# Kernel tuning notes

Hardware: AMD Instinct MI355X
Metric: run time of the kernel (lower is better)

Reference implementation:

```python
import jax, jax.numpy as jnp
import numpy as np

N_HEAD = 16

def setup_inputs() -> dict:
    key = jax.random.key(0)
    ks = jax.random.split(key, 6)
    B, S, T, D = 4, 1024, 576, 1024
    std = 0.02
    return {
        "x": jax.random.normal(ks[0], (B, S, D), jnp.float32),
        "encoder_output": jax.random.normal(ks[1], (B, T, D), jnp.float32),
        "w_attn": jax.random.normal(ks[2], (D, 3 * D), jnp.float32) * std,
        "b_attn": jnp.zeros((3 * D,), jnp.float32),
        "w_vis": jax.random.normal(ks[3], (D, D), jnp.float32) * std,
        "b_vis": jnp.zeros((D,), jnp.float32),
        "w_proj": jax.random.normal(ks[4], (D, D), jnp.float32) * std,
        "b_proj": jnp.zeros((D,), jnp.float32),
    }

def _split_heads(t):
    # [B, L, D] -> [B, H, L, d_head]
    B, L, D = t.shape
    return t.reshape(B, L, N_HEAD, D // N_HEAD).transpose(0, 2, 1, 3)

def reference(x, encoder_output, w_attn, b_attn, w_vis, b_vis, w_proj, b_proj):
    B, S, D = x.shape
    # c_attn: qkv projection of text; only q is actually used downstream
    qkv = x @ w_attn + b_attn                      # [B, S, 3D]
    q = _split_heads(qkv[..., :D])                 # [B, H, S, dh]
    # visual_proj: single projection used as BOTH key and value
    enc = encoder_output @ w_vis + b_vis           # [B, T, D]
    kv = _split_heads(enc)                         # [B, H, T, dh]
    dh = D // N_HEAD
    # scaled dot-product cross-attention (scale=True -> / sqrt(d_head))
    w = jnp.einsum("bhsd,bhtd->bhst", q, kv) / jnp.sqrt(jnp.float32(dh))
    w = jax.nn.softmax(w, axis=-1)                 # attn_dropout=0 (eval)
    a = jnp.einsum("bhst,bhtd->bhsd", w, kv)       # [B, H, S, dh]
    a = a.transpose(0, 2, 1, 3).reshape(B, S, D)   # merge heads
    out = a @ w_proj + b_proj                      # resid_dropout=0 (eval)
    return out
```

## Files before the change

### kernel.cpp

```cpp
#include <hip/hip_runtime.h>
#include <math.h>

#define D_MODEL 1024
#define NHEAD   16
#define DH      64
#define BATCH   4
#define SEQ     1024
#define TKV     576
#define MQ      (BATCH * SEQ)
#define MKV     (BATCH * TKV)
#define NT      (TKV / 64)

typedef __attribute__((ext_vector_type(8))) short bf16x8;
typedef __attribute__((ext_vector_type(4))) float f32x4;

__device__ __forceinline__ unsigned short f2bf(float x) {
    unsigned int u = __float_as_uint(x);
    unsigned int r = (u + 0x7FFFu + ((u >> 16) & 1u)) >> 16;
    return (unsigned short)r;
}
__device__ __forceinline__ float bf2f(unsigned short b) {
    return __uint_as_float((unsigned int)b << 16);
}
__device__ __forceinline__ void split2(float x, unsigned short& h, unsigned short& l) {
    h = f2bf(x);
    l = f2bf(x - bf2f(h));
}

__device__ __forceinline__ void async_copy16(const void* g, void* l) {
    auto gp = (const __attribute__((address_space(1))) unsigned int*)(g);
    auto lp = (__attribute__((address_space(3))) unsigned int*)(l);
    __builtin_amdgcn_global_load_lds(gp, lp, 16, 0, 0);
}

__global__ __launch_bounds__(256) void split_rm(
    const float* __restrict__ in,
    unsigned short* __restrict__ oh, unsigned short* __restrict__ ol)
{
    const size_t i = (size_t)blockIdx.x * 256 + threadIdx.x;
    const float4 v = reinterpret_cast<const float4*>(in)[i];
    ushort4 h, l;
    split2(v.x, h.x, l.x);
    split2(v.y, h.y, l.y);
    split2(v.z, h.z, l.z);
    split2(v.w, h.w, l.w);
    reinterpret_cast<ushort4*>(oh)[i] = h;
    reinterpret_cast<ushort4*>(ol)[i] = l;
}

__global__ __launch_bounds__(256) void split_tr(
    const float* __restrict__ W, int ld,
    unsigned short* __restrict__ th, unsigned short* __restrict__ tl)
{
    __shared__ float sh[32][33];
    const int k0 = blockIdx.x * 32;
    const int n0 = blockIdx.y * 32;
    const int t  = threadIdx.x;
    const int r  = t >> 3;
    const int c4 = (t & 7) * 4;

    const float4 v = *reinterpret_cast<const float4*>(&W[(size_t)(k0 + r) * ld + n0 + c4]);
    sh[r][c4 + 0] = v.x;
    sh[r][c4 + 1] = v.y;
    sh[r][c4 + 2] = v.z;
    sh[r][c4 + 3] = v.w;
    __syncthreads();

    ushort4 h, l;
    split2(sh[c4 + 0][r], h.x, l.x);
    split2(sh[c4 + 1][r], h.y, l.y);
    split2(sh[c4 + 2][r], h.z, l.z);
    split2(sh[c4 + 3][r], h.w, l.w);
    *reinterpret_cast<ushort4*>(&th[(size_t)(n0 + r) * 1024 + k0 + c4]) = h;
    *reinterpret_cast<ushort4*>(&tl[(size_t)(n0 + r) * 1024 + k0 + c4]) = l;
}

__global__ __launch_bounds__(256) void transpose_hl(
    const unsigned short* __restrict__ kvh, const unsigned short* __restrict__ kvl,
    unsigned short* __restrict__ kvth, unsigned short* __restrict__ kvtl)
{
    __shared__ __align__(16) unsigned short th_[64][72];
    __shared__ __align__(16) unsigned short tl_[64][72];
    const int tid = threadIdx.x;
    const int t0  = blockIdx.x * 64;
    const int bh  = blockIdx.y;
    const int b   = bh >> 4;
    const int h   = bh & 15;

#pragma unroll
    for (int p = 0; p < 2; ++p) {
        const int idx = p * 256 + tid;
        const int rr  = idx >> 3;
        const int c   = idx & 7;
        const size_t src = (size_t)(b * TKV + t0 + rr) * 1024 + h * DH + c * 8;
        const bf16x8 vh = *(const bf16x8*)&kvh[src];
        const bf16x8 vl = *(const bf16x8*)&kvl[src];
#pragma unroll
        for (int e = 0; e < 8; ++e) {
            th_[c * 8 + e][rr] = (unsigned short)vh[e];
            tl_[c * 8 + e][rr] = (unsigned short)vl[e];
        }
    }
    __syncthreads();

#pragma unroll
    for (int p = 0; p < 2; ++p) {
        const int idx = p * 256 + tid;
        const int d   = idx >> 3;
        const int c2  = idx & 7;
        const size_t dst = (size_t)(bh * 64 + d) * TKV + t0 + c2 * 8;
        *(bf16x8*)&kvth[dst] = *(const bf16x8*)&th_[d][c2 * 8];
        *(bf16x8*)&kvtl[dst] = *(const bf16x8*)&tl_[d][c2 * 8];
    }
}

template<bool BF16OUT>
__global__ __launch_bounds__(256) void gemm_split_mfma(
    const unsigned short* __restrict__ Ah, const unsigned short* __restrict__ Al,
    const unsigned short* __restrict__ Bth, const unsigned short* __restrict__ Btl,
    const float* __restrict__ bias,
    float* __restrict__ C,
    unsigned short* __restrict__ Ch, unsigned short* __restrict__ Cl,
    int M)
{
    __shared__ unsigned short lds[2][16384];

    const int tid  = threadIdx.x;
    const int lane = tid & 63;
    const int wv   = tid >> 6;

    const int nwg = (gridDim.y << 3);
    const int lin = blockIdx.y * 8 + blockIdx.x;
    const int cpx = nwg >> 3;
    const int swz = (lin & 7) * cpx + (lin >> 3);
    const int brow = (swz >> 3) * 128;
    const int bcol = (swz & 7) * 128;

    const int wr = (wv >> 1) * 64;
    const int wc = (wv & 1) * 64;
    const int lr = lane & 15;
    const int kg = lane >> 4;

    f32x4 acc[4][4];
#pragma unroll
    for (int i = 0; i < 4; ++i)
#pragma unroll
        for (int j = 0; j < 4; ++j) acc[i][j] = (f32x4){0.f, 0.f, 0.f, 0.f};

    auto stage = [&](int buf, int k0) {
#pragma unroll
        for (int i = 0; i < 2; ++i) {
            const int ci = i * 256 + tid;
            const int r  = ci >> 2;
            const int c  = ci & 3;
            const size_t aoff = (size_t)(brow + r) * 1024 + k0 + c * 8;
            const size_t boff = (size_t)(bcol + r) * 1024 + k0 + c * 8;
            char* ldst = (char*)&lds[buf][0] + i * 4096 + wv * 1024;
            async_copy16(Ah  + aoff, ldst);
            async_copy16(Al  + aoff, ldst + 8192);
            async_copy16(Bth + boff, ldst + 16384);
            async_copy16(Btl + boff, ldst + 24576);
        }
    };

    stage(0, 0);
    __syncthreads();

    int cur = 0;
    for (int kt = 0; kt < 32; ++kt) {
        stage(cur ^ 1, ((kt + 1) & 31) << 5);

        const unsigned short* lAh = lds[cur];
        const unsigned short* lAl = lds[cur] + 4096;
        const unsigned short* lBh = lds[cur] + 8192;
        const unsigned short* lBl = lds[cur] + 12288;

        bf16x8 afh[4], afl[4], bfh[4], bfl[4];
#pragma unroll
        for (int f = 0; f < 4; ++f) {
            const int mb = (wr + f * 16 + lr) * 64 + kg * 16;
            const int nb = (wc + f * 16 + lr) * 64 + kg * 16;
            afh[f] = *(const bf16x8*)((const char*)lAh + mb);
            afl[f] = *(const bf16x8*)((const char*)lAl + mb);
            bfh[f] = *(const bf16x8*)((const char*)lBh + nb);
            bfl[f] = *(const bf16x8*)((const char*)lBl + nb);
        }

#pragma unroll
        for (int mf = 0; mf < 4; ++mf)
#pragma unroll
            for (int nf = 0; nf < 4; ++nf) {
                acc[mf][nf] = __builtin_amdgcn_mfma_f32_16x16x32_bf16(afh[mf], bfh[nf], acc[mf][nf], 0, 0, 0);
                acc[mf][nf] = __builtin_amdgcn_mfma_f32_16x16x32_bf16(afh[mf], bfl[nf], acc[mf][nf], 0, 0, 0);
                acc[mf][nf] = __builtin_amdgcn_mfma_f32_16x16x32_bf16(afl[mf], bfh[nf], acc[mf][nf], 0, 0, 0);
            }
        __syncthreads();
        cur ^= 1;
    }

#pragma unroll
    for (int mf = 0; mf < 4; ++mf)
#pragma unroll
        for (int nf = 0; nf < 4; ++nf)
#pragma unroll
            for (int j = 0; j < 4; ++j) {
                const int row = brow + wr + mf * 16 + kg * 4 + j;
                const int col = bcol + wc + nf * 16 + lr;
                const float v = acc[mf][nf][j] + bias[col];
                if constexpr (BF16OUT) {
                    unsigned short hh, ll;
                    split2(v, hh, ll);
                    Ch[(size_t)row * 1024 + col] = hh;
                    Cl[(size_t)row * 1024 + col] = ll;
                } else {
                    C[(size_t)row * 1024 + col] = v;
                }
            }
}

__global__ __launch_bounds__(256, 2) void attn_mfma(
    const unsigned short* __restrict__ qh, const unsigned short* __restrict__ ql,
    const unsigned short* __restrict__ kvh, const unsigned short* __restrict__ kvl,
    const unsigned short* __restrict__ kvth, const unsigned short* __restrict__ kvtl,
    unsigned short* __restrict__ ah, unsigned short* __restrict__ al)
{
    __shared__ __align__(16) unsigned short kh_s[64][64],  kl_s[64][64];
    __shared__ __align__(16) unsigned short vth_s[64][64], vtl_s[64][64];
    __shared__ __align__(16) unsigned short ph_s[4][32][64], pl_s[4][32][64];

    const int tid  = threadIdx.x;
    const int lane = tid & 63;
    const int w    = tid >> 6;
    const int lr   = lane & 15;
    const int kg   = lane >> 4;
    const int s0   = blockIdx.x * 128;
    const int bh   = blockIdx.y;
    const int b    = bh >> 4;
    const int h    = bh & 15;

    const int r0 = tid >> 3;
    const int c0 = tid & 7;

    bf16x8 qhf[2][2], qlf[2][2];
#pragma unroll
    for (int g = 0; g < 2; ++g) {
        const size_t qoff = (size_t)(b * SEQ + s0 + w * 32 + g * 16 + lr) * 1024 + h * DH;
#pragma unroll
        for (int c = 0; c < 2; ++c) {
            qhf[g][c] = *(const bf16x8*)&qh[qoff + c * 32 + kg * 8];
            qlf[g][c] = *(const bf16x8*)&ql[qoff + c * 32 + kg * 8];
        }
    }

    f32x4 oacc[2][4];
#pragma unroll
    for (int g = 0; g < 2; ++g)
#pragma unroll
        for (int nf = 0; nf < 4; ++nf) oacc[g][nf] = (f32x4){0.f, 0.f, 0.f, 0.f};
    float m2[2][4], lsum[2][4];
#pragma unroll
    for (int g = 0; g < 2; ++g)
#pragma unroll
        for (int j = 0; j < 4; ++j) { m2[g][j] = -INFINITY; lsum[g][j] = 0.f; }

    bf16x8 nkh[2], nkl[2], nvh[2], nvl[2];

    auto ld_tile = [&](int it) {
#pragma unroll
        for (int i = 0; i < 2; ++i) {
            const int rr = r0 + i * 32;
            const size_t kvo = (size_t)(b * TKV + it * 64 + rr) * 1024 + h * DH + c0 * 8;
            const size_t vto = (size_t)(bh * 64 + rr) * TKV + it * 64 + c0 * 8;
            nkh[i] = *(const bf16x8*)&kvh[kvo];
            nkl[i] = *(const bf16x8*)&kvl[kvo];
            nvh[i] = *(const bf16x8*)&kvth[vto];
            nvl[i] = *(const bf16x8*)&kvtl[vto];
        }
    };
    auto st_tile = [&]() {
#pragma unroll
        for (int i = 0; i < 2; ++i) {
            const int rr = r0 + i * 32;
            const int sc = (c0 ^ (rr & 7)) * 8;
            *(bf16x8*)&kh_s[rr][sc]  = nkh[i];
            *(bf16x8*)&kl_s[rr][sc]  = nkl[i];
            *(bf16x8*)&vth_s[rr][sc] = nvh[i];
            *(bf16x8*)&vtl_s[rr][sc] = nvl[i];
        }
    };

    ld_tile(0);
    st_tile();
    __syncthreads();

    const float SC2 = 0.125f * 1.44269504089f;

    for (int it = 0; it < NT; ++it) {
        if (it + 1 < NT) ld_tile(it + 1);

        f32x4 sacc[2][4];
#pragma unroll
        for (int g = 0; g < 2; ++g)
#pragma unroll
            for (int nf = 0; nf < 4; ++nf) sacc[g][nf] = (f32x4){0.f, 0.f, 0.f, 0.f};
#pragma unroll
        for (int c = 0; c < 2; ++c) {
            const int ch = (((c << 2) | kg) ^ (lr & 7)) << 3;
#pragma unroll
            for (int nf = 0; nf < 4; ++nf) {
                const bf16x8 bhf = *(const bf16x8*)&kh_s[nf * 16 + lr][ch];
                const bf16x8 blf = *(const bf16x8*)&kl_s[nf * 16 + lr][ch];
#pragma unroll
                for (int g = 0; g < 2; ++g) {
                    sacc[g][nf] = __builtin_amdgcn_mfma_f32_16x16x32_bf16(qhf[g][c], bhf, sacc[g][nf], 0, 0, 0);
                    sacc[g][nf] = __builtin_amdgcn_mfma_f32_16x16x32_bf16(qhf[g][c], blf, sacc[g][nf], 0, 0, 0);
                    sacc[g][nf] = __builtin_amdgcn_mfma_f32_16x16x32_bf16(qlf[g][c], bhf, sacc[g][nf], 0, 0, 0);
                }
            }
        }

#pragma unroll
        for (int g = 0; g < 2; ++g)
#pragma unroll
            for (int j = 0; j < 4; ++j) {
                const float s0v = sacc[g][0][j] * SC2;
                const float s1v = sacc[g][1][j] * SC2;
                const float s2v = sacc[g][2][j] * SC2;
                const float s3v = sacc[g][3][j] * SC2;
                float mx = fmaxf(fmaxf(s0v, s1v), fmaxf(s2v, s3v));
                mx = fmaxf(mx, __shfl_xor(mx, 1));
                mx = fmaxf(mx, __shfl_xor(mx, 2));
                mx = fmaxf(mx, __shfl_xor(mx, 4));
                mx = fmaxf(mx, __shfl_xor(mx, 8));
                const float mnew = fmaxf(m2[g][j], mx);
                const float corr = exp2f(m2[g][j] - mnew);
                const float p0 = exp2f(s0v - mnew);
                const float p1 = exp2f(s1v - mnew);
                const float p2 = exp2f(s2v - mnew);
                const float p3 = exp2f(s3v - mnew);
                float ps = p0 + p1 + p2 + p3;
                ps += __shfl_xor(ps, 1);
                ps += __shfl_xor(ps, 2);
                ps += __shfl_xor(ps, 4);
                ps += __shfl_xor(ps, 8);
                lsum[g][j] = lsum[g][j] * corr + ps;
                m2[g][j] = mnew;
#pragma unroll
                for (int nf = 0; nf < 4; ++nf) oacc[g][nf][j] *= corr;
                const int prow = g * 16 + kg * 4 + j;
                const int key  = prow & 7;
                const int lo3  = lr & 7;
                const int hi1  = lr >> 3;
                unsigned short hh, ll;
                split2(p0, hh, ll);
                ph_s[w][prow][((0 + hi1) ^ key) * 8 + lo3] = hh;
                pl_s[w][prow][((0 + hi1) ^ key) * 8 + lo3] = ll;
                split2(p1, hh, ll);
                ph_s[w][prow][((2 + hi1) ^ key) * 8 + lo3] = hh;
                pl_s[w][prow][((2 + hi1) ^ key) * 8 + lo3] = ll;
                split2(p2, hh, ll);
                ph_s[w][prow][((4 + hi1) ^ key) * 8 + lo3] = hh;
                pl_s[w][prow][((4 + hi1) ^ key) * 8 + lo3] = ll;
                split2(p3, hh, ll);
                ph_s[w][prow][((6 + hi1) ^ key) * 8 + lo3] = hh;
                pl_s[w][prow][((6 + hi1) ^ key) * 8 + lo3] = ll;
            }

#pragma unroll
        for (int c = 0; c < 2; ++c) {
            const int ch = (((c << 2) | kg) ^ (lr & 7)) << 3;
            bf16x8 pha[2], pla[2];
#pragma unroll
            for (int g = 0; g < 2; ++g) {
                pha[g] = *(const bf16x8*)&ph_s[w][g * 16 + lr][ch];
                pla[g] = *(const bf16x8*)&pl_s[w][g * 16 + lr][ch];
            }
#pragma unroll
            for (int nf = 0; nf < 4; ++nf) {
                const bf16x8 vhf = *(const bf16x8*)&vth_s[nf * 16 + lr][ch];
                const bf16x8 vlf = *(const bf16x8*)&vtl_s[nf * 16 + lr][ch];
#pragma unroll
                for (int g = 0; g < 2; ++g) {
                    oacc[g][nf] = __builtin_amdgcn_mfma_f32_16x16x32_bf16(pha[g], vhf, oacc[g][nf], 0, 0, 0);
                    oacc[g][nf] = __builtin_amdgcn_mfma_f32_16x16x32_bf16(pha[g], vlf, oacc[g][nf], 0, 0, 0);
                    oacc[g][nf] = __builtin_amdgcn_mfma_f32_16x16x32_bf16(pla[g], vhf, oacc[g][nf], 0, 0, 0);
                }
            }
        }

        __syncthreads();
        if (it + 1 < NT) st_tile();
        __syncthreads();
    }

#pragma unroll
    for (int g = 0; g < 2; ++g)
#pragma unroll
        for (int nf = 0; nf < 4; ++nf)
#pragma unroll
            for (int j = 0; j < 4; ++j) {
                const float v = oacc[g][nf][j] / lsum[g][j];
                const int srow = b * SEQ + s0 + w * 32 + g * 16 + kg * 4 + j;
                const int col  = h * DH + nf * 16 + lr;
                unsigned short hh, ll;
                split2(v, hh, ll);
                ah[(size_t)srow * 1024 + col] = hh;
                al[(size_t)srow * 1024 + col] = ll;
            }
}

extern "C" void kernel_launch(void* const* d_in, const int* in_sizes, int n_in,
                              void* d_out, int out_size, void* d_ws, size_t ws_size,
                              hipStream_t stream)
{
    const float* x      = (const float*)d_in[0];
    const float* enc    = (const float*)d_in[1];
    const float* w_attn = (const float*)d_in[2];
    const float* b_attn = (const float*)d_in[3];
    const float* w_vis  = (const float*)d_in[4];
    const float* b_vis  = (const float*)d_in[5];
    const float* w_proj = (const float*)d_in[6];
    const float* b_proj = (const float*)d_in[7];
    float* out = (float*)d_out;

    char* base = (char*)d_ws;
    unsigned short* xh   = (unsigned short*)(base + 0);
    unsigned short* xl   = (unsigned short*)(base + 8388608);
    unsigned short* ench = (unsigned short*)(base + 16777216);
    unsigned short* encl = (unsigned short*)(base + 21495808);
    unsigned short* w1h  = (unsigned short*)(base + 26214400);
    unsigned short* w1l  = (unsigned short*)(base + 28311552);
    unsigned short* w2h  = (unsigned short*)(base + 30408704);
    unsigned short* w2l  = (unsigned short*)(base + 32505856);
    unsigned short* w3h  = (unsigned short*)(base + 34603008);
    unsigned short* w3l  = (unsigned short*)(base + 36700160);
    unsigned short* qh   = (unsigned short*)(base + 38797312);
    unsigned short* ql   = (unsigned short*)(base + 47185920);
    unsigned short* kvh  = (unsigned short*)(base + 55574528);
    unsigned short* kvl  = (unsigned short*)(base + 60293120);
    unsigned short* kvth = (unsigned short*)(base + 0);
    unsigned short* kvtl = (unsigned short*)(base + 4718592);
    unsigned short* atth = (unsigned short*)(base + 16777216);
    unsigned short* attl = (unsigned short*)(base + 26214400);

    split_rm<<<(MQ  * 1024 / 4) / 256, 256, 0, stream>>>(x, xh, xl);
    split_rm<<<(MKV * 1024 / 4) / 256, 256, 0, stream>>>(enc, ench, encl);
    split_tr<<<dim3(32, 32), 256, 0, stream>>>(w_attn, 3 * D_MODEL, w1h, w1l);
    split_tr<<<dim3(32, 32), 256, 0, stream>>>(w_vis,  D_MODEL, w2h, w2l);
    split_tr<<<dim3(32, 32), 256, 0, stream>>>(w_proj, D_MODEL, w3h, w3l);

    gemm_split_mfma<true><<<dim3(8, MQ / 128), 256, 0, stream>>>(
        xh, xl, w1h, w1l, b_attn, nullptr, qh, ql, MQ);
    gemm_split_mfma<true><<<dim3(8, MKV / 128), 256, 0, stream>>>(
        ench, encl, w2h, w2l, b_vis, nullptr, kvh, kvl, MKV);
    transpose_hl<<<dim3(TKV / 64, BATCH * NHEAD), 256, 0, stream>>>(kvh, kvl, kvth, kvtl);
    attn_mfma<<<dim3(SEQ / 128, BATCH * NHEAD), 256, 0, stream>>>(
        qh, ql, kvh, kvl, kvth, kvtl, atth, attl);
    gemm_split_mfma<false><<<dim3(8, MQ / 128), 256, 0, stream>>>(
        atth, attl, w3h, w3l, b_proj, out, nullptr, nullptr, MQ);
}
```

Before: 284.9 us.

## Merge Q/KV projection GEMMs and restructure attention with async LDS staging

Merges the Q and KV projection GEMMs into a single launch so the two fill the GPU together instead of running back to back. The attention kernel is rewritten to stage K and V tiles into LDS with async copies, using a pre-permuted V layout built by the transpose kernel. It computes S^T so softmax probabilities stay in registers instead of going through LDS, and raises occupancy to 3 blocks per CU by shrinking shared memory. The cost is more complex indexing, extra syncs per tile, and a serialized K/V staging order that may expose latency.

```diff
diff --git a/kernel.cpp b/kernel.cpp
--- a/kernel.cpp
+++ b/kernel.cpp
@@ -75,14 +75,15 @@
     *reinterpret_cast<ushort4*>(&tl[(size_t)(n0 + r) * 1024 + k0 + c4]) = l;
 }
 
-__global__ __launch_bounds__(256) void transpose_hl(
+__global__ __launch_bounds__(256) void transpose_perm(
     const unsigned short* __restrict__ kvh, const unsigned short* __restrict__ kvl,
-    unsigned short* __restrict__ kvth, unsigned short* __restrict__ kvtl)
+    unsigned short* __restrict__ vph, unsigned short* __restrict__ vpl)
 {
     __shared__ __align__(16) unsigned short th_[64][72];
     __shared__ __align__(16) unsigned short tl_[64][72];
     const int tid = threadIdx.x;
-    const int t0  = blockIdx.x * 64;
+    const int it  = blockIdx.x;
+    const int t0  = it * 64;
     const int bh  = blockIdx.y;
     const int b   = bh >> 4;
     const int h   = bh & 15;
@@ -107,35 +108,35 @@
     for (int p = 0; p < 2; ++p) {
         const int idx = p * 256 + tid;
         const int d   = idx >> 3;
-        const int c2  = idx & 7;
-        const size_t dst = (size_t)(bh * 64 + d) * TKV + t0 + c2 * 8;
-        *(bf16x8*)&kvth[dst] = *(const bf16x8*)&th_[d][c2 * 8];
-        *(bf16x8*)&kvtl[dst] = *(const bf16x8*)&tl_[d][c2 * 8];
+        const int lc  = idx & 7;
+        const int q   = lc >> 2;
+        const int kg  = lc & 3;
+        const ushort4 a  = *(const ushort4*)&th_[d][32 * q + kg * 4];
+        const ushort4 bb = *(const ushort4*)&th_[d][32 * q + 16 + kg * 4];
+        const ushort4 a2  = *(const ushort4*)&tl_[d][32 * q + kg * 4];
+        const ushort4 bb2 = *(const ushort4*)&tl_[d][32 * q + 16 + kg * 4];
+        bf16x8 oh_, ol_;
+        oh_[0] = (short)a.x;  oh_[1] = (short)a.y;  oh_[2] = (short)a.z;  oh_[3] = (short)a.w;
+        oh_[4] = (short)bb.x; oh_[5] = (short)bb.y; oh_[6] = (short)bb.z; oh_[7] = (short)bb.w;
+        ol_[0] = (short)a2.x;  ol_[1] = (short)a2.y;  ol_[2] = (short)a2.z;  ol_[3] = (short)a2.w;
+        ol_[4] = (short)bb2.x; ol_[5] = (short)bb2.y; ol_[6] = (short)bb2.z; ol_[7] = (short)bb2.w;
+        const size_t dst = ((size_t)(bh * 64 + d) * NT + it) * 64 + lc * 8;
+        *(bf16x8*)&vph[dst] = oh_;
+        *(bf16x8*)&vpl[dst] = ol_;
     }
 }
 
 template<bool BF16OUT>
-__global__ __launch_bounds__(256) void gemm_split_mfma(
-    const unsigned short* __restrict__ Ah, const unsigned short* __restrict__ Al,
-    const unsigned short* __restrict__ Bth, const unsigned short* __restrict__ Btl,
-    const float* __restrict__ bias,
-    float* __restrict__ C,
-    unsigned short* __restrict__ Ch, unsigned short* __restrict__ Cl,
-    int M)
-{
-    __shared__ unsigned short lds[2][16384];
-
+__device__ __forceinline__ void gemm_body(
+    const unsigned short* Ah, const unsigned short* Al,
+    const unsigned short* Bth, const unsigned short* Btl,
+    const float* bias, float* C,
+    unsigned short* Ch, unsigned short* Cl,
+    int brow, int bcol, unsigned short* lds )
+{
     const int tid  = threadIdx.x;
     const int lane = tid & 63;
     const int wv   = tid >> 6;
-
-    const int nwg = (gridDim.y << 3);
-    const int lin = blockIdx.y * 8 + blockIdx.x;
-    const int cpx = nwg >> 3;
-    const int swz = (lin & 7) * cpx + (lin >> 3);
-    const int brow = (swz >> 3) * 128;
-    const int bcol = (swz & 7) * 128;
-
     const int wr = (wv >> 1) * 64;
     const int wc = (wv & 1) * 64;
     const int lr = lane & 15;
@@ -155,7 +156,7 @@
             const int c  = ci & 3;
             const size_t aoff = (size_t)(brow + r) * 1024 + k0 + c * 8;
             const size_t boff = (size_t)(bcol + r) * 1024 + k0 + c * 8;
-            char* ldst = (char*)&lds[buf][0] + i * 4096 + wv * 1024;
+            char* ldst = (char*)lds + buf * 32768 + i * 4096 + wv * 1024;
             async_copy16(Ah  + aoff, ldst);
             async_copy16(Al  + aoff, ldst + 8192);
             async_copy16(Bth + boff, ldst + 16384);
@@ -170,10 +171,10 @@
     for (int kt = 0; kt < 32; ++kt) {
         stage(cur ^ 1, ((kt + 1) & 31) << 5);
 
-        const unsigned short* lAh = lds[cur];
-        const unsigned short* lAl = lds[cur] + 4096;
-        const unsigned short* lBh = lds[cur] + 8192;
-        const unsigned short* lBl = lds[cur] + 12288;
+        const unsigned short* lAh = lds + cur * 16384;
+        const unsigned short* lAl = lAh + 4096;
+        const unsigned short* lBh = lAh + 8192;
+        const unsigned short* lBl = lAh + 12288;
 
         bf16x8 afh[4], afl[4], bfh[4], bfl[4];
 #pragma unroll
@@ -218,15 +219,53 @@
             }
 }
 
-__global__ __launch_bounds__(256, 2) void attn_mfma(
+__global__ __launch_bounds__(256) void gemm_split_mfma_f32(
+    const unsigned short* __restrict__ Ah, const unsigned short* __restrict__ Al,
+    const unsigned short* __restrict__ Bth, const unsigned short* __restrict__ Btl,
+    const float* __restrict__ bias, float* __restrict__ C)
+{
+    __shared__ unsigned short lds[2 * 16384];
+    const int nwg = (gridDim.y << 3);
+    const int lin = blockIdx.y * 8 + blockIdx.x;
+    const int cpx = nwg >> 3;
+    const int swz = (lin & 7) * cpx + (lin >> 3);
+    gemm_body<false>(Ah, Al, Bth, Btl, bias, C, nullptr, nullptr,
+                     (swz >> 3) * 128, (swz & 7) * 128, lds);
+}
+
+__global__ __launch_bounds__(256) void gemm12_split_mfma(
+    const unsigned short* __restrict__ A1h, const unsigned short* __restrict__ A1l,
+    const unsigned short* __restrict__ B1h, const unsigned short* __restrict__ B1l,
+    const float* __restrict__ bias1,
+    unsigned short* __restrict__ C1h, unsigned short* __restrict__ C1l,
+    const unsigned short* __restrict__ A2h, const unsigned short* __restrict__ A2l,
+    const unsigned short* __restrict__ B2h, const unsigned short* __restrict__ B2l,
+    const float* __restrict__ bias2,
+    unsigned short* __restrict__ C2h, unsigned short* __restrict__ C2l)
+{
+    __shared__ unsigned short lds[2 * 16384];
+    const int nwg = (gridDim.y << 3);
+    const int lin = blockIdx.y * 8 + blockIdx.x;
+    const int cpx = nwg >> 3;
+    const int swz = (lin & 7) * cpx + (lin >> 3);
+    const int ridx = swz >> 3;
+    const int bcol = (swz & 7) * 128;
+    if (ridx < 32) {
+        gemm_body<true>(A1h, A1l, B1h, B1l, bias1, nullptr, C1h, C1l,
+                        ridx * 128, bcol, lds);
+    } else {
+        gemm_body<true>(A2h, A2l, B2h, B2l, bias2, nullptr, C2h, C2l,
+                        (ridx - 32) * 128, bcol, lds);
+    }
+}
+
+__global__ __launch_bounds__(256, 3) void attn_mfma(
     const unsigned short* __restrict__ qh, const unsigned short* __restrict__ ql,
     const unsigned short* __restrict__ kvh, const unsigned short* __restrict__ kvl,
-    const unsigned short* __restrict__ kvth, const unsigned short* __restrict__ kvtl,
+    const unsigned short* __restrict__ vph, const unsigned short* __restrict__ vpl,
     unsigned short* __restrict__ ah, unsigned short* __restrict__ al)
 {
-    __shared__ __align__(16) unsigned short kh_s[64][64],  kl_s[64][64];
-    __shared__ __align__(16) unsigned short vth_s[64][64], vtl_s[64][64];
-    __shared__ __align__(16) unsigned short ph_s[4][32][64], pl_s[4][32][64];
+    __shared__ __align__(16) unsigned short smem[4 * 4096];
 
     const int tid  = threadIdx.x;
     const int lane = tid & 63;
@@ -237,9 +276,31 @@
     const int bh   = blockIdx.y;
     const int b    = bh >> 4;
     const int h    = bh & 15;
-
-    const int r0 = tid >> 3;
-    const int c0 = tid & 7;
+    const int rr0  = tid >> 3;
+    const int cc   = tid & 7;
+
+    auto stageK = [&](int it) {
+#pragma unroll
+        for (int i = 0; i < 2; ++i) {
+            const int rr = rr0 + i * 32;
+            const int lc = cc ^ (rr & 7);
+            const size_t src = (size_t)(b * TKV + it * 64 + rr) * 1024 + h * DH + lc * 8;
+            char* dst = (char*)smem + i * 4096 + w * 1024;
+            async_copy16(kvh + src, dst);
+            async_copy16(kvl + src, dst + 8192);
+        }
+    };
+    auto stageV = [&](int it) {
+#pragma unroll
+        for (int i = 0; i < 2; ++i) {
+            const int rr = rr0 + i * 32;
+            const int lc = cc ^ (rr & 7);
+            const size_t src = ((size_t)(bh * 64 + rr) * NT + it) * 64 + lc * 8;
+            char* dst = (char*)smem + 16384 + i * 4096 + w * 1024;
+            async_copy16(vph + src, dst);
+            async_copy16(vpl + src, dst + 8192);
+        }
+    };
 
     bf16x8 qhf[2][2], qlf[2][2];
 #pragma unroll
@@ -256,157 +317,117 @@
 #pragma unroll
     for (int g = 0; g < 2; ++g)
 #pragma unroll
-        for (int nf = 0; nf < 4; ++nf) oacc[g][nf] = (f32x4){0.f, 0.f, 0.f, 0.f};
-    float m2[2][4], lsum[2][4];
-#pragma unroll
-    for (int g = 0; g < 2; ++g)
-#pragma unroll
-        for (int j = 0; j < 4; ++j) { m2[g][j] = -INFINITY; lsum[g][j] = 0.f; }
-
-    bf16x8 nkh[2], nkl[2], nvh[2], nvl[2];
-
-    auto ld_tile = [&](int it) {
-#pragma unroll
-        for (int i = 0; i < 2; ++i) {
-            const int rr = r0 + i * 32;
-            const size_t kvo = (size_t)(b * TKV + it * 64 + rr) * 1024 + h * DH + c0 * 8;
-            const size_t vto = (size_t)(bh * 64 + rr) * TKV + it * 64 + c0 * 8;
-            nkh[i] = *(const bf16x8*)&kvh[kvo];
-            nkl[i] = *(const bf16x8*)&kvl[kvo];
-            nvh[i] = *(const bf16x8*)&kvth[vto];
-            nvl[i] = *(const bf16x8*)&kvtl[vto];
-        }
-    };
-    auto st_tile = [&]() {
-#pragma unroll
-        for (int i = 0; i < 2; ++i) {
-            const int rr = r0 + i * 32;
-            const int sc = (c0 ^ (rr & 7)) * 8;
-            *(bf16x8*)&kh_s[rr][sc]  = nkh[i];
-            *(bf16x8*)&kl_s[rr][sc]  = nkl[i];
-            *(bf16x8*)&vth_s[rr][sc] = nvh[i];
-            *(bf16x8*)&vtl_s[rr][sc] = nvl[i];
-        }
-    };
-
-    ld_tile(0);
-    st_tile();
+        for (int df = 0; df < 4; ++df) oacc[g][df] = (f32x4){0.f, 0.f, 0.f, 0.f};
+    float m2[2]   = {-INFINITY, -INFINITY};
+    float lsum[2] = {0.f, 0.f};
+
+    stageK(0);
+    stageV(0);
     __syncthreads();
 
     const float SC2 = 0.125f * 1.44269504089f;
 
     for (int it = 0; it < NT; ++it) {
-        if (it + 1 < NT) ld_tile(it + 1);
-
         f32x4 sacc[2][4];
 #pragma unroll
         for (int g = 0; g < 2; ++g)
 #pragma unroll
-            for (int nf = 0; nf < 4; ++nf) sacc[g][nf] = (f32x4){0.f, 0.f, 0.f, 0.f};
-#pragma unroll
-        for (int c = 0; c < 2; ++c) {
-            const int ch = (((c << 2) | kg) ^ (lr & 7)) << 3;
-#pragma unroll
-            for (int nf = 0; nf < 4; ++nf) {
-                const bf16x8 bhf = *(const bf16x8*)&kh_s[nf * 16 + lr][ch];
-                const bf16x8 blf = *(const bf16x8*)&kl_s[nf * 16 + lr][ch];
+            for (int kf = 0; kf < 4; ++kf) sacc[g][kf] = (f32x4){0.f, 0.f, 0.f, 0.f};
+#pragma unroll
+        for (int c = 0; c < 2; ++c)
+#pragma unroll
+            for (int kf = 0; kf < 4; ++kf) {
+                const int ka = (kf * 16 + lr) * 128 + ((((c << 2) | kg) ^ (lr & 7)) << 4);
+                const bf16x8 akh = *(const bf16x8*)((const char*)smem + ka);
+                const bf16x8 akl = *(const bf16x8*)((const char*)smem + 8192 + ka);
 #pragma unroll
                 for (int g = 0; g < 2; ++g) {
-                    sacc[g][nf] = __builtin_amdgcn_mfma_f32_16x16x32_bf16(qhf[g][c], bhf, sacc[g][nf], 0, 0, 0);
-                    sacc[g][nf] = __builtin_amdgcn_mfma_f32_16x16x32_bf16(qhf[g][c], blf, sacc[g][nf], 0, 0, 0);
-                    sacc[g][nf] = __builtin_amdgcn_mfma_f32_16x16x32_bf16(qlf[g][c], bhf, sacc[g][nf], 0, 0, 0);
+                    sacc[g][kf] = __builtin_amdgcn_mfma_f32_16x16x32_bf16(akh, qhf[g][c], sacc[g][kf], 0, 0, 0);
+                    sacc[g][kf] = __builtin_amdgcn_mfma_f32_16x16x32_bf16(akh, qlf[g][c], sacc[g][kf], 0, 0, 0);
+                    sacc[g][kf] = __builtin_amdgcn_mfma_f32_16x16x32_bf16(akl, qhf[g][c], sacc[g][kf], 0, 0, 0);
                 }
             }
-        }
-
-#pragma unroll
-        for (int g = 0; g < 2; ++g)
+
+        __syncthreads();
+        if (it + 1 < NT) stageK(it + 1);
+
+        bf16x8 pbh[2][2], pbl[2][2];
+#pragma unroll
+        for (int g = 0; g < 2; ++g) {
+            float p[16];
+            float mx = -INFINITY;
+#pragma unroll
+            for (int kf = 0; kf < 4; ++kf)
+#pragma unroll
+                for (int j = 0; j < 4; ++j) {
+                    p[kf * 4 + j] = sacc[g][kf][j] * SC2;
+                    mx = fmaxf(mx, p[kf * 4 + j]);
+                }
+            mx = fmaxf(mx, __shfl_xor(mx, 16));
+            mx = fmaxf(mx, __shfl_xor(mx, 32));
+            const float mnew = fmaxf(m2[g], mx);
+            const float corr = exp2f(m2[g] - mnew);
+            float ps = 0.f;
+#pragma unroll
+            for (int i = 0; i < 16; ++i) { p[i] = exp2f(p[i] - mnew); ps += p[i]; }
+            ps += __shfl_xor(ps, 16);
+            ps += __shfl_xor(ps, 32);
+            lsum[g] = lsum[g] * corr + ps;
+            m2[g] = mnew;
+#pragma unroll
+            for (int df = 0; df < 4; ++df)
+#pragma unroll
+                for (int j = 0; j < 4; ++j) oacc[g][df][j] *= corr;
+#pragma unroll
+            for (int q = 0; q < 2; ++q) {
+                bf16x8 bh_, bl_;
+#pragma unroll
+                for (int e = 0; e < 8; ++e) {
+                    unsigned short hh, ll;
+                    split2(p[(2 * q + (e >> 2)) * 4 + (e & 3)], hh, ll);
+                    bh_[e] = (short)hh;
+                    bl_[e] = (short)ll;
+                }
+                pbh[g][q] = bh_;
+                pbl[g][q] = bl_;
+            }
+        }
+
+#pragma unroll
+        for (int q = 0; q < 2; ++q)
+#pragma unroll
+            for (int df = 0; df < 4; ++df) {
+                const int va = (df * 16 + lr) * 128 + ((((q << 2) | kg) ^ (lr & 7)) << 4);
+                const bf16x8 avh = *(const bf16x8*)((const char*)smem + 16384 + va);
+                const bf16x8 avl = *(const bf16x8*)((const char*)smem + 24576 + va);
+#pragma unroll
+                for (int g = 0; g < 2; ++g) {
+                    oacc[g][df] = __builtin_amdgcn_mfma_f32_16x16x32_bf16(avh, pbh[g][q], oacc[g][df], 0, 0, 0);
+                    oacc[g][df] = __builtin_amdgcn_mfma_f32_16x16x32_bf16(avh, pbl[g][q], oacc[g][df], 0, 0, 0);
+                    oacc[g][df] = __builtin_amdgcn_mfma_f32_16x16x32_bf16(avl, pbh[g][q], oacc[g][df], 0, 0, 0);
+                }
+            }
+
+        __syncthreads();
+        if (it + 1 < NT) stageV(it + 1);
+    }
+
+#pragma unroll
+    for (int g = 0; g < 2; ++g) {
+        const float rinv = 1.f / lsum[g];
+        const int srow = b * SEQ + s0 + w * 32 + g * 16 + lr;
+#pragma unroll
+        for (int df = 0; df < 4; ++df)
 #pragma unroll
             for (int j = 0; j < 4; ++j) {
-                const float s0v = sacc[g][0][j] * SC2;
-                const float s1v = sacc[g][1][j] * SC2;
-                const float s2v = sacc[g][2][j] * SC2;
-                const float s3v = sacc[g][3][j] * SC2;
-                float mx = fmaxf(fmaxf(s0v, s1v), fmaxf(s2v, s3v));
-                mx = fmaxf(mx, __shfl_xor(mx, 1));
-                mx = fmaxf(mx, __shfl_xor(mx, 2));
-                mx = fmaxf(mx, __shfl_xor(mx, 4));
-                mx = fmaxf(mx, __shfl_xor(mx, 8));
-                const float mnew = fmaxf(m2[g][j], mx);
-                const float corr = exp2f(m2[g][j] - mnew);
-                const float p0 = exp2f(s0v - mnew);
-                const float p1 = exp2f(s1v - mnew);
-                const float p2 = exp2f(s2v - mnew);
-                const float p3 = exp2f(s3v - mnew);
-                float ps = p0 + p1 + p2 + p3;
-                ps += __shfl_xor(ps, 1);
-                ps += __shfl_xor(ps, 2);
-                ps += __shfl_xor(ps, 4);
-                ps += __shfl_xor(ps, 8);
-                lsum[g][j] = lsum[g][j] * corr + ps;
-                m2[g][j] = mnew;
-#pragma unroll
-                for (int nf = 0; nf < 4; ++nf) oacc[g][nf][j] *= corr;
-                const int prow = g * 16 + kg * 4 + j;
-                const int key  = prow & 7;
-                const int lo3  = lr & 7;
-                const int hi1  = lr >> 3;
-                unsigned short hh, ll;
-                split2(p0, hh, ll);
-                ph_s[w][prow][((0 + hi1) ^ key) * 8 + lo3] = hh;
-                pl_s[w][prow][((0 + hi1) ^ key) * 8 + lo3] = ll;
-                split2(p1, hh, ll);
-                ph_s[w][prow][((2 + hi1) ^ key) * 8 + lo3] = hh;
-                pl_s[w][prow][((2 + hi1) ^ key) * 8 + lo3] = ll;
-                split2(p2, hh, ll);
-                ph_s[w][prow][((4 + hi1) ^ key) * 8 + lo3] = hh;
-                pl_s[w][prow][((4 + hi1) ^ key) * 8 + lo3] = ll;
-                split2(p3, hh, ll);
-                ph_s[w][prow][((6 + hi1) ^ key) * 8 + lo3] = hh;
-                pl_s[w][prow][((6 + hi1) ^ key) * 8 + lo3] = ll;
-            }
-
-#pragma unroll
-        for (int c = 0; c < 2; ++c) {
-            const int ch = (((c << 2) | kg) ^ (lr & 7)) << 3;
-            bf16x8 pha[2], pla[2];
-#pragma unroll
-            for (int g = 0; g < 2; ++g) {
-                pha[g] = *(const bf16x8*)&ph_s[w][g * 16 + lr][ch];
-                pla[g] = *(const bf16x8*)&pl_s[w][g * 16 + lr][ch];
-            }
-#pragma unroll
-            for (int nf = 0; nf < 4; ++nf) {
-                const bf16x8 vhf = *(const bf16x8*)&vth_s[nf * 16 + lr][ch];
-                const bf16x8 vlf = *(const bf16x8*)&vtl_s[nf * 16 + lr][ch];
-#pragma unroll
-                for (int g = 0; g < 2; ++g) {
-                    oacc[g][nf] = __builtin_amdgcn_mfma_f32_16x16x32_bf16(pha[g], vhf, oacc[g][nf], 0, 0, 0);
-                    oacc[g][nf] = __builtin_amdgcn_mfma_f32_16x16x32_bf16(pha[g], vlf, oacc[g][nf], 0, 0, 0);
-                    oacc[g][nf] = __builtin_amdgcn_mfma_f32_16x16x32_bf16(pla[g], vhf, oacc[g][nf], 0, 0, 0);
-                }
-            }
-        }
-
-        __syncthreads();
-        if (it + 1 < NT) st_tile();
-        __syncthreads();
-    }
-
-#pragma unroll
-    for (int g = 0; g < 2; ++g)
-#pragma unroll
-        for (int nf = 0; nf < 4; ++nf)
-#pragma unroll
-            for (int j = 0; j < 4; ++j) {
-                const float v = oacc[g][nf][j] / lsum[g][j];
-                const int srow = b * SEQ + s0 + w * 32 + g * 16 + kg * 4 + j;
-                const int col  = h * DH + nf * 16 + lr;
+                const float v = oacc[g][df][j] * rinv;
+                const int col = h * DH + df * 16 + kg * 4 + j;
                 unsigned short hh, ll;
                 split2(v, hh, ll);
                 ah[(size_t)srow * 1024 + col] = hh;
                 al[(size_t)srow * 1024 + col] = ll;
             }
+    }
 }
 
 extern "C" void kernel_launch(void* const* d_in, const int* in_sizes, int n_in,
@@ -438,8 +459,8 @@
     unsigned short* ql   = (unsigned short*)(base + 47185920);
     unsigned short* kvh  = (unsigned short*)(base + 55574528);
     unsigned short* kvl  = (unsigned short*)(base + 60293120);
-    unsigned short* kvth = (unsigned short*)(base + 0);
-    unsigned short* kvtl = (unsigned short*)(base + 4718592);
+    unsigned short* vph  = (unsigned short*)(base + 0);
+    unsigned short* vpl  = (unsigned short*)(base + 4718592);
     unsigned short* atth = (unsigned short*)(base + 16777216);
     unsigned short* attl = (unsigned short*)(base + 26214400);
 
@@ -449,13 +470,12 @@
     split_tr<<<dim3(32, 32), 256, 0, stream>>>(w_vis,  D_MODEL, w2h, w2l);
     split_tr<<<dim3(32, 32), 256, 0, stream>>>(w_proj, D_MODEL, w3h, w3l);
 
-    gemm_split_mfma<true><<<dim3(8, MQ / 128), 256, 0, stream>>>(
-        xh, xl, w1h, w1l, b_attn, nullptr, qh, ql, MQ);
-    gemm_split_mfma<true><<<dim3(8, MKV / 128), 256, 0, stream>>>(
-        ench, encl, w2h, w2l, b_vis, nullptr, kvh, kvl, MKV);
-    transpose_hl<<<dim3(TKV / 64, BATCH * NHEAD), 256, 0, stream>>>(kvh, kvl, kvth, kvtl);
+    gemm12_split_mfma<<<dim3(8, 50), 256, 0, stream>>>(
+        xh, xl, w1h, w1l, b_attn, qh, ql,
+        ench, encl, w2h, w2l, b_vis, kvh, kvl);
+    transpose_perm<<<dim3(NT, BATCH * NHEAD), 256, 0, stream>>>(kvh, kvl, vph, vpl);
     attn_mfma<<<dim3(SEQ / 128, BATCH * NHEAD), 256, 0, stream>>>(
-        qh, ql, kvh, kvl, kvth, kvtl, atth, attl);
-    gemm_split_mfma<false><<<dim3(8, MQ / 128), 256, 0, stream>>>(
-        atth, attl, w3h, w3l, b_proj, out, nullptr, nullptr, MQ);
-}
+        qh, ql, kvh, kvl, vph, vpl, atth, attl);
+    gemm_split_mfma_f32<<<dim3(8, MQ / 128), 256, 0, stream>>>(
+        atth, attl, w3h, w3l, b_proj, out);
+}
```

Result: faster. 242.0 us (-15.0%).
